# Performance work log

Measured on AMD Instinct MI355X. Metric: run time of the kernel, lower is better.

The kernel has to match this reference:

```python
import jax, jax.numpy as jnp
import numpy as np

B, C, H, W = 4, 256, 48, 48
HEADS, DH = 8, 64
HID = HEADS * DH
EPS = 1e-5
SCALE = DH ** -0.5


def setup_inputs() -> dict:
    key = jax.random.key(0)
    ks = jax.random.split(key, 8)
    return {
        "tensor": jax.random.normal(ks[0], (B, C, H, W), jnp.float32),
        "norm_g": jnp.ones((C,), jnp.float32),                      # ChanLayerNorm gamma
        "w_qkv": jax.random.normal(ks[1], (3 * HID, C), jnp.float32) * 0.02,  # 1x1 conv, no bias
        "dw_q": jax.random.normal(ks[2], (HID, 1, 3, 3), jnp.float32) * 0.1,  # depthwise 3x3
        "dw_k": jax.random.normal(ks[3], (HID, 1, 3, 3), jnp.float32) * 0.1,
        "dw_v": jax.random.normal(ks[4], (HID, 1, 3, 3), jnp.float32) * 0.1,
        "w_out": jax.random.normal(ks[5], (C, HID), jnp.float32) * 0.02,      # 1x1 conv out
        "b_out": jnp.zeros((C,), jnp.float32),
    }


def _rope(t):
    # t: (b, h, s, d) -- rotary embedding over flattened spatial positions
    s, d = t.shape[-2], t.shape[-1]
    inv_freq = 1.0 / (10000.0 ** (jnp.arange(0, d, 2, dtype=jnp.float32) / d))
    freqs = jnp.arange(s, dtype=jnp.float32)[:, None] * inv_freq[None, :]     # (s, d/2)
    emb = jnp.concatenate([freqs, freqs], axis=-1)                            # (s, d)
    cos, sin = jnp.cos(emb), jnp.sin(emb)
    t1, t2 = t[..., : d // 2], t[..., d // 2 :]
    rot = jnp.concatenate([-t2, t1], axis=-1)
    return t * cos + rot * sin


def _dwconv(x, w):
    # depthwise 3x3, padding=1 (Primer conv), groups = channels
    return jax.lax.conv_general_dilated(
        x, w, window_strides=(1, 1), padding="SAME",
        feature_group_count=x.shape[1],
        dimension_numbers=("NCHW", "OIHW", "NCHW"))


def reference(tensor, norm_g, w_qkv, dw_q, dw_k, dw_v, w_out, b_out):
    x = tensor
    # ChanLayerNorm: normalize over channel dim
    mean = jnp.mean(x, axis=1, keepdims=True)
    var = jnp.var(x, axis=1, keepdims=True)
    xn = (x - mean) * jax.lax.rsqrt(var + EPS) * norm_g[None, :, None, None]
    # 1x1 conv to qkv
    qkv = jnp.einsum("bchw,oc->bohw", xn, w_qkv)
    q, k, v = jnp.split(qkv, 3, axis=1)
    q, k, v = _dwconv(q, dw_q), _dwconv(k, dw_k), _dwconv(v, dw_v)
    # b (h d) x y -> b h (x y) d
    def to_seq(t):
        b = t.shape[0]
        return t.reshape(b, HEADS, DH, H * W).transpose(0, 1, 3, 2)
    q, k, v = to_seq(q), to_seq(k), to_seq(v)
    q, k = _rope(q), _rope(k)
    q = q * SCALE
    sim = jnp.einsum("bhid,bhjd->bhij", q, k)
    attn = jax.nn.softmax(sim, axis=-1)
    out = jnp.einsum("bhij,bhjd->bhid", attn, v)
    # b h (x y) d -> b (h d) x y
    out = out.transpose(0, 1, 3, 2).reshape(out.shape[0], HID, H, W)
    return jnp.einsum("bchw,oc->bohw", out, w_out) + b_out[None, :, None, None]
```

## Files before the change

kernel.cpp:

```cpp
#include <hip/hip_runtime.h>
#include <math.h>

#define SS 2304
#define C_IN 256
#define HID 512
#define QKV3 1536
#define HEADS 8
#define DH 64
#define BATCH 4
#define EPSV 1e-5f
#define SCALEV 0.125f

typedef short s8v __attribute__((ext_vector_type(8)));
typedef float f4v __attribute__((ext_vector_type(4)));
typedef unsigned int u4v __attribute__((ext_vector_type(4)));
typedef unsigned int uint32;

static __device__ inline unsigned short f2bf(float x) {
    unsigned int u = __float_as_uint(x);
    u += 0x7fffu + ((u >> 16) & 1u);
    return (unsigned short)(u >> 16);
}
static __device__ inline float bf2f(unsigned short h) {
    return __uint_as_float((unsigned int)h << 16);
}
static __device__ inline f4v mm(s8v a, s8v b, f4v c) {
    return __builtin_amdgcn_mfma_f32_16x16x32_bf16(a, b, c, 0, 0, 0);
}
static __device__ inline s8v pk4(uint32 a, uint32 b, uint32 c, uint32 d) {
    u4v t; t[0] = a; t[1] = b; t[2] = c; t[3] = d;
    return __builtin_bit_cast(s8v, t);
}
static __device__ inline uint32 pk_rnd(float x) {
    unsigned int u = __float_as_uint(x);
    unsigned int uh = (u + (0x7fffu + ((u >> 16) & 1u))) & 0xffff0000u;
    float r = x - __uint_as_float(uh);
    return (uh >> 16) | (__float_as_uint(r) & 0xffff0000u);
}
static __device__ inline uint32 pk_trunc(float x) {
    unsigned int u = __float_as_uint(x);
    unsigned int h = u & 0xffff0000u;
    float r = x - __uint_as_float(h);
    return (h >> 16) | (__float_as_uint(r) & 0xffff0000u);
}
static __device__ inline uint32 rot16(uint32 u) { return (u >> 16) | (u << 16); }
static __device__ inline u4v rot16v(u4v u) {
    u4v r; r[0] = rot16(u[0]); r[1] = rot16(u[1]); r[2] = rot16(u[2]); r[3] = rot16(u[3]);
    return r;
}

__global__ void prep_wgint(const float* __restrict__ w, const float* __restrict__ g,
                           uint32* __restrict__ wgint, float* __restrict__ wsum) {
    __shared__ float red[256];
    int o = blockIdx.x, c = threadIdx.x;
    float v = w[o * C_IN + c] * g[c];
    wgint[o * C_IN + c] = pk_rnd(v);
    red[c] = v;
    __syncthreads();
    for (int st = 128; st > 0; st >>= 1) {
        if (c < st) red[c] += red[c + st];
        __syncthreads();
    }
    if (c == 0) wsum[o] = red[0];
}

__global__ void prep_woutint(const float* __restrict__ w, uint32* __restrict__ wi) {
    int idx = blockIdx.x * 256 + threadIdx.x;
    wi[idx] = pk_rnd(w[idx]);
}

__global__ void prep_rope(float* __restrict__ cosT, float* __restrict__ sinT) {
    int idx = blockIdx.x * 256 + threadIdx.x;
    if (idx >= SS * 32) return;
    int s = idx >> 5, f = idx & 31;
    double inv = pow(10000.0, -(double)f / 32.0);
    double ang = (double)s * inv;
    cosT[idx] = (float)cos(ang);
    sinT[idx] = (float)sin(ang);
}

__global__ __launch_bounds__(256) void xt_pack(const float* __restrict__ x,
                                               uint32* __restrict__ xTint,
                                               float* __restrict__ psum,
                                               float* __restrict__ psq) {
    __shared__ float tile[64][65];
    __shared__ float sred[4][64];
    __shared__ float qred[4][64];
    int b = blockIdx.z;
    int c0 = blockIdx.y * 64;
    int s0 = blockIdx.x * 64;
    int t = threadIdx.x;
    int sl = t & 63, cg = t >> 6;
    float ps = 0.f, pq = 0.f;
#pragma unroll
    for (int i = 0; i < 16; ++i) {
        int c = cg * 16 + i;
        float v = x[((size_t)b * C_IN + c0 + c) * SS + s0 + sl];
        tile[c][sl] = v;
        ps += v;
        pq += v * v;
    }
    sred[cg][sl] = ps;
    qred[cg][sl] = pq;
    __syncthreads();
    int cl = t & 63, sg = t >> 6;
#pragma unroll
    for (int i = 0; i < 16; ++i) {
        int s = sg * 16 + i;
        xTint[((size_t)b * SS + s0 + s) * C_IN + c0 + cl] = pk_rnd(tile[cl][s]);
    }
    if (t < 64) {
        float S = (sred[0][t] + sred[1][t]) + (sred[2][t] + sred[3][t]);
        float Q = (qred[0][t] + qred[1][t]) + (qred[2][t] + qred[3][t]);
        size_t o = (size_t)blockIdx.y * (BATCH * SS) + (size_t)b * SS + s0 + t;
        psum[o] = S;
        psq[o] = Q;
    }
}

__global__ void finalize_stats(const float* __restrict__ psum,
                               const float* __restrict__ psq,
                               float* __restrict__ mean, float* __restrict__ rstd) {
    int p = blockIdx.x * 256 + threadIdx.x;
    const int NP = BATCH * SS;
    float S = (psum[p] + psum[NP + p]) + (psum[2 * NP + p] + psum[3 * NP + p]);
    float Q = (psq[p] + psq[NP + p]) + (psq[2 * NP + p] + psq[3 * NP + p]);
    float mu = S * (1.0f / C_IN);
    float var = Q * (1.0f / C_IN) - mu * mu;
    mean[p] = mu;
    rstd[p] = rsqrtf(var + EPSV);
}

__global__ __launch_bounds__(256, 4) void qkv_mfma(
    const uint32* __restrict__ wgint, const uint32* __restrict__ xTint,
    const float* __restrict__ wsum, const float* __restrict__ mean,
    const float* __restrict__ rstd, float* __restrict__ qkv) {
    int b = blockIdx.z;
    int m0 = blockIdx.y * 128;
    int n0 = blockIdx.x * 64;
    int t = threadIdx.x;
    int wv = t >> 6, lane = t & 63, l15 = lane & 15, quad = lane >> 4;
    int wm = wv * 32;
    const uint32* Ab = wgint + (size_t)(m0 + wm) * C_IN;
    const uint32* Bb = xTint + ((size_t)b * SS + n0) * C_IN;
    f4v acc[2][4];
#pragma unroll
    for (int mt = 0; mt < 2; ++mt)
#pragma unroll
        for (int nt = 0; nt < 4; ++nt) acc[mt][nt] = (f4v){0.f, 0.f, 0.f, 0.f};
    u4v af[2][2], bf[2][4];
    auto ldA = [&](int ch, u4v* A) {
#pragma unroll
        for (int mt = 0; mt < 2; ++mt)
            A[mt] = *(const u4v*)(Ab + (size_t)(mt * 16 + l15) * C_IN + ch * 16 + quad * 4);
    };
    auto ldB = [&](int ch, u4v* B) {
#pragma unroll
        for (int nt = 0; nt < 4; ++nt)
            B[nt] = *(const u4v*)(Bb + (size_t)(nt * 16 + l15) * C_IN + ch * 16 + quad * 4);
    };
    ldA(0, af[0]);
    ldB(0, bf[0]);
#pragma unroll 2
    for (int ch = 0; ch < 16; ++ch) {
        int cur = ch & 1, nxt = cur ^ 1;
        if (ch + 1 < 16) { ldA(ch + 1, af[nxt]); ldB(ch + 1, bf[nxt]); }
        u4v br[4];
#pragma unroll
        for (int nt = 0; nt < 4; ++nt) br[nt] = rot16v(bf[cur][nt]);
#pragma unroll
        for (int mt = 0; mt < 2; ++mt) {
            s8v a = __builtin_bit_cast(s8v, af[cur][mt]);
#pragma unroll
            for (int nt = 0; nt < 4; ++nt) {
                acc[mt][nt] = mm(a, __builtin_bit_cast(s8v, bf[cur][nt]), acc[mt][nt]);
                acc[mt][nt] = mm(a, __builtin_bit_cast(s8v, br[nt]), acc[mt][nt]);
            }
        }
    }
    float mnv[4], rsv[4];
#pragma unroll
    for (int nt = 0; nt < 4; ++nt) {
        int n = n0 + nt * 16 + l15;
        mnv[nt] = mean[b * SS + n];
        rsv[nt] = rstd[b * SS + n];
    }
#pragma unroll
    for (int mt = 0; mt < 2; ++mt)
#pragma unroll
        for (int r = 0; r < 4; ++r) {
            int m = m0 + wm + mt * 16 + quad * 4 + r;
            float ws = wsum[m];
            float* dst = qkv + ((size_t)b * QKV3 + m) * SS + n0 + l15;
#pragma unroll
            for (int nt = 0; nt < 4; ++nt)
                dst[nt * 16] = rsv[nt] * (acc[mt][nt][r] - mnv[nt] * ws);
        }
}

__global__ __launch_bounds__(256) void conv_rope(
    const float* __restrict__ qkv, const float* __restrict__ dwq,
    const float* __restrict__ dwk, const float* __restrict__ dwv,
    const float* __restrict__ cosT, const float* __restrict__ sinT,
    unsigned short* __restrict__ qhi, unsigned short* __restrict__ qlo,
    unsigned short* __restrict__ khi, unsigned short* __restrict__ klo,
    uint32* __restrict__ vtint) {
    __shared__ float tile[64][65];
    int b = blockIdx.z;
    int part = blockIdx.y >> 3;
    int h = blockIdx.y & 7;
    int s0 = blockIdx.x * 64;
    int t = threadIdx.x;
    int sl = t & 63, dgrp = t >> 6;
    int s = s0 + sl;
    int y = s / 48, xx = s - y * 48;
    int bh = b * HEADS + h;
    const float* dw = (part == 0) ? dwq : (part == 1) ? dwk : dwv;
#pragma unroll
    for (int i = 0; i < 16; ++i) {
        int d = dgrp * 16 + i;
        int cch = part * HID + h * DH + d;
        const float* src = qkv + ((size_t)b * QKV3 + cch) * SS;
        const float* wp = dw + (h * DH + d) * 9;
        float acc = 0.f;
#pragma unroll
        for (int dy = -1; dy <= 1; ++dy) {
            int yy = y + dy;
            if (yy < 0 || yy >= 48) continue;
#pragma unroll
            for (int dx = -1; dx <= 1; ++dx) {
                int xv = xx + dx;
                if (xv < 0 || xv >= 48) continue;
                acc += wp[(dy + 1) * 3 + (dx + 1)] * src[yy * 48 + xv];
            }
        }
        if (part == 2) {
            size_t o = ((size_t)bh * DH + d) * SS + s;
            vtint[o] = pk_rnd(acc);
        } else {
            tile[d][sl] = acc;
        }
    }
    if (part == 2) return;
    __syncthreads();
    int d2 = t & 63, srow = t >> 6;
    unsigned short* hiA = (part == 0) ? qhi : khi;
    unsigned short* loA = (part == 0) ? qlo : klo;
#pragma unroll
    for (int i = 0; i < 16; ++i) {
        int sp = srow + 4 * i;
        float v0 = tile[d2][sp];
        float vp = tile[d2 ^ 32][sp];
        int f = d2 & 31;
        float cv = cosT[(s0 + sp) * 32 + f];
        float sv = sinT[(s0 + sp) * 32 + f];
        float rot = (d2 < 32) ? -vp : vp;
        float val = v0 * cv + rot * sv;
        if (part == 0) val *= SCALEV;
        size_t o = ((size_t)bh * SS + s0 + sp) * DH + d2;
        unsigned short hu = f2bf(val);
        hiA[o] = hu;
        loA[o] = f2bf(val - bf2f(hu));
    }
}

__global__ __launch_bounds__(256, 2) void attn_mfma(
    const unsigned short* __restrict__ qhi, const unsigned short* __restrict__ qlo,
    const unsigned short* __restrict__ khi, const unsigned short* __restrict__ klo,
    const uint32* __restrict__ vtint,
    float* __restrict__ Opart, float* __restrict__ lpart) {
    __shared__ float lds[2][64][68];
    __shared__ float lsl[4][64];
    int bh = blockIdx.z;
    int jh = blockIdx.y;
    int i0 = blockIdx.x * 64;
    int t = threadIdx.x;
    int wv = t >> 6;
    int lane = t & 63;
    int l15 = lane & 15;
    int quad = lane >> 4;

    s8v qf[4][4];
#pragma unroll
    for (int ig = 0; ig < 4; ++ig) {
        size_t qb = ((size_t)bh * SS + i0 + ig * 16 + l15) * DH + quad * 8;
        qf[ig][0] = *(const s8v*)(qhi + qb);
        qf[ig][1] = *(const s8v*)(qhi + qb + 32);
        qf[ig][2] = *(const s8v*)(qlo + qb);
        qf[ig][3] = *(const s8v*)(qlo + qb + 32);
    }
    f4v oacc[4][4];
#pragma unroll
    for (int dt = 0; dt < 4; ++dt)
#pragma unroll
        for (int ig = 0; ig < 4; ++ig) oacc[dt][ig] = (f4v){0.f, 0.f, 0.f, 0.f};
    float lsum[4] = {0.f, 0.f, 0.f, 0.f};

    const size_t kbh = (size_t)bh * SS * DH;
    const uint32* vbase = vtint + (size_t)bh * DH * SS;
    const int jbase = jh * 1152 + wv * 16;

    s8v kc[2][4], vc[2][4];
    auto ldK = [&](int s, s8v* K) {
        size_t row = kbh + (size_t)(jbase + s * 64 + l15) * DH + quad * 8;
        K[0] = *(const s8v*)(khi + row);
        K[1] = *(const s8v*)(khi + row + 32);
        K[2] = *(const s8v*)(klo + row);
        K[3] = *(const s8v*)(klo + row + 32);
    };
    auto ldV = [&](int s, s8v* V) {
        size_t col = (size_t)(jbase + s * 64 + quad * 4);
#pragma unroll
        for (int dt = 0; dt < 4; ++dt)
            V[dt] = __builtin_bit_cast(
                s8v, *(const u4v*)(vbase + (size_t)(dt * 16 + l15) * SS + col));
    };
    ldK(0, kc[0]);
    ldV(0, vc[0]);
#pragma unroll 2
    for (int s = 0; s < 18; ++s) {
        int cur = s & 1, nxt = cur ^ 1;
        if (s + 1 < 18) { ldK(s + 1, kc[nxt]); ldV(s + 1, vc[nxt]); }
        f4v sv[4];
#pragma unroll
        for (int ig = 0; ig < 4; ++ig) {
            f4v sx = {0.f, 0.f, 0.f, 0.f};
            sx = mm(kc[cur][0], qf[ig][0], sx);
            sx = mm(kc[cur][1], qf[ig][1], sx);
            sx = mm(kc[cur][0], qf[ig][2], sx);
            sx = mm(kc[cur][1], qf[ig][3], sx);
            sx = mm(kc[cur][2], qf[ig][0], sx);
            sx = mm(kc[cur][3], qf[ig][1], sx);
            sv[ig] = sx;
        }
        s8v B1[4], B2[4];
#pragma unroll
        for (int ig = 0; ig < 4; ++ig) {
            float p0 = __expf(sv[ig][0]), p1 = __expf(sv[ig][1]);
            float p2 = __expf(sv[ig][2]), p3 = __expf(sv[ig][3]);
            lsum[ig] += (p0 + p1) + (p2 + p3);
            uint32 u0 = pk_trunc(p0), u1 = pk_trunc(p1);
            uint32 u2 = pk_trunc(p2), u3 = pk_trunc(p3);
            B1[ig] = pk4(u0, u1, u2, u3);
            B2[ig] = pk4(rot16(u0), rot16(u1), rot16(u2), rot16(u3));
        }
#pragma unroll
        for (int dt = 0; dt < 4; ++dt)
#pragma unroll
            for (int ig = 0; ig < 4; ++ig) {
                oacc[dt][ig] = mm(vc[cur][dt], B1[ig], oacc[dt][ig]);
                oacc[dt][ig] = mm(vc[cur][dt], B2[ig], oacc[dt][ig]);
            }
    }
#pragma unroll
    for (int ig = 0; ig < 4; ++ig) {
        float v = lsum[ig];
        v += __shfl_xor(v, 16);
        v += __shfl_xor(v, 32);
        if (quad == 0) lsl[wv][ig * 16 + l15] = v;
    }
    if (wv < 2) {
#pragma unroll
        for (int dt = 0; dt < 4; ++dt)
#pragma unroll
            for (int ig = 0; ig < 4; ++ig)
#pragma unroll
                for (int r = 0; r < 4; ++r)
                    lds[wv][dt * 16 + quad * 4 + r][ig * 16 + l15] = oacc[dt][ig][r];
    }
    __syncthreads();
    if (wv >= 2) {
#pragma unroll
        for (int dt = 0; dt < 4; ++dt)
#pragma unroll
            for (int ig = 0; ig < 4; ++ig)
#pragma unroll
                for (int r = 0; r < 4; ++r)
                    lds[wv - 2][dt * 16 + quad * 4 + r][ig * 16 + l15] += oacc[dt][ig][r];
    }
    __syncthreads();
    int d = t >> 2, qg = (t & 3) * 16;
    size_t ob = (((size_t)jh * 32 + bh) * DH + d) * SS + i0 + qg;
#pragma unroll
    for (int j4 = 0; j4 < 4; ++j4) {
        float4 a0 = *(const float4*)&lds[0][d][qg + j4 * 4];
        float4 a1 = *(const float4*)&lds[1][d][qg + j4 * 4];
        float4 rr;
        rr.x = a0.x + a1.x;
        rr.y = a0.y + a1.y;
        rr.z = a0.z + a1.z;
        rr.w = a0.w + a1.w;
        *(float4*)(Opart + ob + j4 * 4) = rr;
    }
    if (t < 64) {
        float v = (lsl[0][t] + lsl[1][t]) + (lsl[2][t] + lsl[3][t]);
        lpart[((size_t)jh * 32 + bh) * SS + i0 + t] = v;
    }
}

__global__ __launch_bounds__(256) void combine_t(
    const float* __restrict__ Opart, const float* __restrict__ lpart,
    uint32* __restrict__ OTint) {
    __shared__ uint32 tile[64][65];
    int bh = blockIdx.y;
    int s0 = blockIdx.x * 64;
    int b = bh >> 3, h = bh & 7;
    int t = threadIdx.x;
    int sl = t & 63, dg = t >> 6;
    float linv = 1.f / (lpart[(size_t)bh * SS + s0 + sl] +
                        lpart[(size_t)(32 + bh) * SS + s0 + sl]);
#pragma unroll
    for (int i = 0; i < 16; ++i) {
        int d = dg * 16 + i;
        size_t off = ((size_t)bh * DH + d) * SS + s0 + sl;
        float v = (Opart[off] + Opart[off + (size_t)32 * DH * SS]) * linv;
        tile[d][sl] = pk_rnd(v);
    }
    __syncthreads();
    int dl = t & 63, sg = t >> 6;
#pragma unroll
    for (int i = 0; i < 16; ++i) {
        int s = sg * 16 + i;
        OTint[((size_t)b * SS + s0 + s) * HID + h * DH + dl] = tile[dl][s];
    }
}

__global__ __launch_bounds__(256, 4) void outproj_mfma(
    const uint32* __restrict__ OTint, const uint32* __restrict__ woutint,
    const float* __restrict__ b_out, float* __restrict__ out) {
    int b = blockIdx.z;
    int m0 = blockIdx.y * 32;
    int n0 = blockIdx.x * 128;
    int t = threadIdx.x;
    int wv = t >> 6, lane = t & 63, l15 = lane & 15, quad = lane >> 4;
    int wn = wv * 32;
    const uint32* Ab = woutint + (size_t)m0 * HID;
    const uint32* Bb = OTint + ((size_t)b * SS + n0 + wn) * HID;
    f4v acc[2][2];
#pragma unroll
    for (int mt = 0; mt < 2; ++mt)
#pragma unroll
        for (int nt = 0; nt < 2; ++nt) acc[mt][nt] = (f4v){0.f, 0.f, 0.f, 0.f};
    u4v af[2][2], bf[2][2];
    auto ldA = [&](int ch, u4v* A) {
#pragma unroll
        for (int mt = 0; mt < 2; ++mt)
            A[mt] = *(const u4v*)(Ab + (size_t)(mt * 16 + l15) * HID + ch * 16 + quad * 4);
    };
    auto ldB = [&](int ch, u4v* B) {
#pragma unroll
        for (int nt = 0; nt < 2; ++nt)
            B[nt] = *(const u4v*)(Bb + (size_t)(nt * 16 + l15) * HID + ch * 16 + quad * 4);
    };
    ldA(0, af[0]);
    ldB(0, bf[0]);
#pragma unroll 2
    for (int ch = 0; ch < 32; ++ch) {
        int cur = ch & 1, nxt = cur ^ 1;
        if (ch + 1 < 32) { ldA(ch + 1, af[nxt]); ldB(ch + 1, bf[nxt]); }
        u4v br[2];
#pragma unroll
        for (int nt = 0; nt < 2; ++nt) br[nt] = rot16v(bf[cur][nt]);
#pragma unroll
        for (int mt = 0; mt < 2; ++mt) {
            s8v a = __builtin_bit_cast(s8v, af[cur][mt]);
#pragma unroll
            for (int nt = 0; nt < 2; ++nt) {
                acc[mt][nt] = mm(a, __builtin_bit_cast(s8v, bf[cur][nt]), acc[mt][nt]);
                acc[mt][nt] = mm(a, __builtin_bit_cast(s8v, br[nt]), acc[mt][nt]);
            }
        }
    }
#pragma unroll
    for (int mt = 0; mt < 2; ++mt)
#pragma unroll
        for (int r = 0; r < 4; ++r) {
            int o = m0 + mt * 16 + quad * 4 + r;
            float bo = b_out[o];
            float* dst = out + ((size_t)b * C_IN + o) * SS + n0 + wn + l15;
#pragma unroll
            for (int nt = 0; nt < 2; ++nt) dst[nt * 16] = acc[mt][nt][r] + bo;
        }
}

extern "C" void kernel_launch(void* const* d_in, const int* in_sizes, int n_in,
                              void* d_out, int out_size, void* d_ws, size_t ws_size,
                              hipStream_t stream) {
    (void)in_sizes; (void)n_in; (void)out_size; (void)ws_size;
    const float* x     = (const float*)d_in[0];
    const float* g     = (const float*)d_in[1];
    const float* w_qkv = (const float*)d_in[2];
    const float* dwq   = (const float*)d_in[3];
    const float* dwk   = (const float*)d_in[4];
    const float* dwv   = (const float*)d_in[5];
    const float* w_out = (const float*)d_in[6];
    const float* b_out = (const float*)d_in[7];
    float* out = (float*)d_out;

    char* ws = (char*)d_ws;
    size_t off = 0;
    auto alloc = [&](size_t nbytes) -> void* {
        char* p = ws + off;
        off = (off + nbytes + 255) & ~(size_t)255;
        return (void*)p;
    };
    const size_t NSD = (size_t)BATCH * HEADS * SS * DH;
    uint32* wgint   = (uint32*)alloc((size_t)QKV3 * C_IN * 4);
    uint32* woutint = (uint32*)alloc((size_t)C_IN * HID * 4);
    float* wsum = (float*)alloc((size_t)QKV3 * 4);
    float* mean = (float*)alloc((size_t)BATCH * SS * 4);
    float* rstd = (float*)alloc((size_t)BATCH * SS * 4);
    float* psum = (float*)alloc((size_t)4 * BATCH * SS * 4);
    float* psq  = (float*)alloc((size_t)4 * BATCH * SS * 4);
    float* cosT = (float*)alloc((size_t)SS * 32 * 4);
    float* sinT = (float*)alloc((size_t)SS * 32 * 4);
    float* qkv  = (float*)alloc((size_t)BATCH * QKV3 * SS * 4);
    unsigned short* qhi  = (unsigned short*)alloc(NSD * 2);
    unsigned short* qlo  = (unsigned short*)alloc(NSD * 2);
    unsigned short* khi  = (unsigned short*)alloc(NSD * 2);
    unsigned short* klo  = (unsigned short*)alloc(NSD * 2);
    uint32* vtint = (uint32*)alloc(NSD * 4);
    float* lpart = (float*)alloc((size_t)2 * 32 * SS * 4);
    uint32* xTint = (uint32*)qhi;
    float*  Opart = qkv;
    uint32* OTint = (uint32*)(qkv + 2 * NSD);

    prep_wgint<<<QKV3, 256, 0, stream>>>(w_qkv, g, wgint, wsum);
    prep_woutint<<<512, 256, 0, stream>>>(w_out, woutint);
    prep_rope<<<288, 256, 0, stream>>>(cosT, sinT);
    xt_pack<<<dim3(36, 4, BATCH), 256, 0, stream>>>(x, xTint, psum, psq);
    finalize_stats<<<36, 256, 0, stream>>>(psum, psq, mean, rstd);
    qkv_mfma<<<dim3(36, 12, BATCH), 256, 0, stream>>>(wgint, xTint, wsum, mean, rstd, qkv);
    conv_rope<<<dim3(36, 24, BATCH), 256, 0, stream>>>(qkv, dwq, dwk, dwv, cosT, sinT,
                                                       qhi, qlo, khi, klo, vtint);
    attn_mfma<<<dim3(36, 2, 32), 256, 0, stream>>>(qhi, qlo, khi, klo, vtint,
                                                   Opart, lpart);
    combine_t<<<dim3(36, 32), 256, 0, stream>>>(Opart, lpart, OTint);
    outproj_mfma<<<dim3(18, 8, BATCH), 256, 0, stream>>>(OTint, woutint, b_out, out);
}
```

Before: 481.1 us.

## Split attention waves into 2x2 query/key groups to cut registers and raise occupancy

Each wave now handles 32 queries over a 32-key slice instead of 64 queries over a 16-key slice, which halves the query fragments and output accumulators held per wave. K/V prefetch changes from a double buffer to single buffers reloaded right after use. Launch bounds rise from 2 to 3 blocks per SM, and LDS use for the reduction shrinks. The aim is higher occupancy to hide latency, at the cost of less explicit load/compute overlap and more K/V loads per query.

New measurement: 670.4 us. 39.4% more time.

```diff
diff --git a/kernel.cpp b/kernel.cpp
--- a/kernel.cpp
+++ b/kernel.cpp
@@ -264,13 +264,13 @@
     }
 }
 
-__global__ __launch_bounds__(256, 2) void attn_mfma(
+__global__ __launch_bounds__(256, 3) void attn_mfma(
     const unsigned short* __restrict__ qhi, const unsigned short* __restrict__ qlo,
     const unsigned short* __restrict__ khi, const unsigned short* __restrict__ klo,
     const uint32* __restrict__ vtint,
     float* __restrict__ Opart, float* __restrict__ lpart) {
-    __shared__ float lds[2][64][68];
-    __shared__ float lsl[4][64];
+    __shared__ float lds[2][64][36];
+    __shared__ float lsl[4][32];
     int bh = blockIdx.z;
     int jh = blockIdx.y;
     int i0 = blockIdx.x * 64;
@@ -279,121 +279,124 @@
     int lane = t & 63;
     int l15 = lane & 15;
     int quad = lane >> 4;
-
-    s8v qf[4][4];
-#pragma unroll
-    for (int ig = 0; ig < 4; ++ig) {
-        size_t qb = ((size_t)bh * SS + i0 + ig * 16 + l15) * DH + quad * 8;
+    int qg = wv >> 1;
+    int ks = wv & 1;
+
+    s8v qf[2][4];
+#pragma unroll
+    for (int ig = 0; ig < 2; ++ig) {
+        size_t qb = ((size_t)bh * SS + i0 + qg * 32 + ig * 16 + l15) * DH + quad * 8;
         qf[ig][0] = *(const s8v*)(qhi + qb);
         qf[ig][1] = *(const s8v*)(qhi + qb + 32);
         qf[ig][2] = *(const s8v*)(qlo + qb);
         qf[ig][3] = *(const s8v*)(qlo + qb + 32);
     }
-    f4v oacc[4][4];
+    f4v oacc[4][2];
 #pragma unroll
     for (int dt = 0; dt < 4; ++dt)
 #pragma unroll
-        for (int ig = 0; ig < 4; ++ig) oacc[dt][ig] = (f4v){0.f, 0.f, 0.f, 0.f};
-    float lsum[4] = {0.f, 0.f, 0.f, 0.f};
+        for (int ig = 0; ig < 2; ++ig) oacc[dt][ig] = (f4v){0.f, 0.f, 0.f, 0.f};
+    float lsum[2] = {0.f, 0.f};
 
     const size_t kbh = (size_t)bh * SS * DH;
     const uint32* vbase = vtint + (size_t)bh * DH * SS;
-    const int jbase = jh * 1152 + wv * 16;
+    const int jb0 = jh * 1152 + ks * 32;
 
     s8v kc[2][4], vc[2][4];
-    auto ldK = [&](int s, s8v* K) {
-        size_t row = kbh + (size_t)(jbase + s * 64 + l15) * DH + quad * 8;
-        K[0] = *(const s8v*)(khi + row);
-        K[1] = *(const s8v*)(khi + row + 32);
-        K[2] = *(const s8v*)(klo + row);
-        K[3] = *(const s8v*)(klo + row + 32);
-    };
-    auto ldV = [&](int s, s8v* V) {
-        size_t col = (size_t)(jbase + s * 64 + quad * 4);
-#pragma unroll
-        for (int dt = 0; dt < 4; ++dt)
-            V[dt] = __builtin_bit_cast(
-                s8v, *(const u4v*)(vbase + (size_t)(dt * 16 + l15) * SS + col));
-    };
-    ldK(0, kc[0]);
-    ldV(0, vc[0]);
-#pragma unroll 2
+    auto ldK = [&](int s) {
+#pragma unroll
+        for (int kt = 0; kt < 2; ++kt) {
+            size_t row = kbh + (size_t)(jb0 + s * 64 + kt * 16 + l15) * DH + quad * 8;
+            kc[kt][0] = *(const s8v*)(khi + row);
+            kc[kt][1] = *(const s8v*)(khi + row + 32);
+            kc[kt][2] = *(const s8v*)(klo + row);
+            kc[kt][3] = *(const s8v*)(klo + row + 32);
+        }
+    };
+    auto ldV = [&](int s) {
+#pragma unroll
+        for (int kt = 0; kt < 2; ++kt) {
+            size_t col = (size_t)(jb0 + s * 64 + kt * 16 + quad * 4);
+#pragma unroll
+            for (int dt = 0; dt < 4; ++dt)
+                vc[kt][dt] = __builtin_bit_cast(
+                    s8v, *(const u4v*)(vbase + (size_t)(dt * 16 + l15) * SS + col));
+        }
+    };
+    ldK(0);
+    ldV(0);
     for (int s = 0; s < 18; ++s) {
-        int cur = s & 1, nxt = cur ^ 1;
-        if (s + 1 < 18) { ldK(s + 1, kc[nxt]); ldV(s + 1, vc[nxt]); }
-        f4v sv[4];
-#pragma unroll
-        for (int ig = 0; ig < 4; ++ig) {
-            f4v sx = {0.f, 0.f, 0.f, 0.f};
-            sx = mm(kc[cur][0], qf[ig][0], sx);
-            sx = mm(kc[cur][1], qf[ig][1], sx);
-            sx = mm(kc[cur][0], qf[ig][2], sx);
-            sx = mm(kc[cur][1], qf[ig][3], sx);
-            sx = mm(kc[cur][2], qf[ig][0], sx);
-            sx = mm(kc[cur][3], qf[ig][1], sx);
-            sv[ig] = sx;
-        }
-        s8v B1[4], B2[4];
-#pragma unroll
-        for (int ig = 0; ig < 4; ++ig) {
-            float p0 = __expf(sv[ig][0]), p1 = __expf(sv[ig][1]);
-            float p2 = __expf(sv[ig][2]), p3 = __expf(sv[ig][3]);
-            lsum[ig] += (p0 + p1) + (p2 + p3);
-            uint32 u0 = pk_trunc(p0), u1 = pk_trunc(p1);
-            uint32 u2 = pk_trunc(p2), u3 = pk_trunc(p3);
-            B1[ig] = pk4(u0, u1, u2, u3);
-            B2[ig] = pk4(rot16(u0), rot16(u1), rot16(u2), rot16(u3));
-        }
-#pragma unroll
-        for (int dt = 0; dt < 4; ++dt)
-#pragma unroll
-            for (int ig = 0; ig < 4; ++ig) {
-                oacc[dt][ig] = mm(vc[cur][dt], B1[ig], oacc[dt][ig]);
-                oacc[dt][ig] = mm(vc[cur][dt], B2[ig], oacc[dt][ig]);
+        f4v sv[2][2];
+#pragma unroll
+        for (int kt = 0; kt < 2; ++kt)
+#pragma unroll
+            for (int ig = 0; ig < 2; ++ig) {
+                f4v sx = {0.f, 0.f, 0.f, 0.f};
+                sx = mm(kc[kt][0], qf[ig][0], sx);
+                sx = mm(kc[kt][1], qf[ig][1], sx);
+                sx = mm(kc[kt][0], qf[ig][2], sx);
+                sx = mm(kc[kt][1], qf[ig][3], sx);
+                sx = mm(kc[kt][2], qf[ig][0], sx);
+                sx = mm(kc[kt][3], qf[ig][1], sx);
+                sv[kt][ig] = sx;
             }
-    }
-#pragma unroll
-    for (int ig = 0; ig < 4; ++ig) {
+        if (s + 1 < 18) ldK(s + 1);
+#pragma unroll
+        for (int kt = 0; kt < 2; ++kt)
+#pragma unroll
+            for (int ig = 0; ig < 2; ++ig) {
+                float p0 = __expf(sv[kt][ig][0]), p1 = __expf(sv[kt][ig][1]);
+                float p2 = __expf(sv[kt][ig][2]), p3 = __expf(sv[kt][ig][3]);
+                lsum[ig] += (p0 + p1) + (p2 + p3);
+                uint32 u0 = pk_trunc(p0), u1 = pk_trunc(p1);
+                uint32 u2 = pk_trunc(p2), u3 = pk_trunc(p3);
+                s8v B1 = pk4(u0, u1, u2, u3);
+                s8v B2 = pk4(rot16(u0), rot16(u1), rot16(u2), rot16(u3));
+#pragma unroll
+                for (int dt = 0; dt < 4; ++dt) {
+                    oacc[dt][ig] = mm(vc[kt][dt], B1, oacc[dt][ig]);
+                    oacc[dt][ig] = mm(vc[kt][dt], B2, oacc[dt][ig]);
+                }
+            }
+        if (s + 1 < 18) ldV(s + 1);
+    }
+#pragma unroll
+    for (int ig = 0; ig < 2; ++ig) {
         float v = lsum[ig];
         v += __shfl_xor(v, 16);
         v += __shfl_xor(v, 32);
         if (quad == 0) lsl[wv][ig * 16 + l15] = v;
     }
-    if (wv < 2) {
+    if (ks == 0) {
 #pragma unroll
         for (int dt = 0; dt < 4; ++dt)
 #pragma unroll
-            for (int ig = 0; ig < 4; ++ig)
+            for (int ig = 0; ig < 2; ++ig)
 #pragma unroll
                 for (int r = 0; r < 4; ++r)
-                    lds[wv][dt * 16 + quad * 4 + r][ig * 16 + l15] = oacc[dt][ig][r];
+                    lds[qg][dt * 16 + quad * 4 + r][ig * 16 + l15] = oacc[dt][ig][r];
     }
     __syncthreads();
-    if (wv >= 2) {
+    if (ks == 1) {
 #pragma unroll
         for (int dt = 0; dt < 4; ++dt)
 #pragma unroll
-            for (int ig = 0; ig < 4; ++ig)
+            for (int ig = 0; ig < 2; ++ig)
 #pragma unroll
                 for (int r = 0; r < 4; ++r)
-                    lds[wv - 2][dt * 16 + quad * 4 + r][ig * 16 + l15] += oacc[dt][ig][r];
+                    lds[qg][dt * 16 + quad * 4 + r][ig * 16 + l15] += oacc[dt][ig][r];
     }
     __syncthreads();
-    int d = t >> 2, qg = (t & 3) * 16;
-    size_t ob = (((size_t)jh * 32 + bh) * DH + d) * SS + i0 + qg;
+    int d = t >> 2, qb4 = (t & 3) * 16;
+    size_t ob = (((size_t)jh * 32 + bh) * DH + d) * SS + i0 + qb4;
 #pragma unroll
     for (int j4 = 0; j4 < 4; ++j4) {
-        float4 a0 = *(const float4*)&lds[0][d][qg + j4 * 4];
-        float4 a1 = *(const float4*)&lds[1][d][qg + j4 * 4];
-        float4 rr;
-        rr.x = a0.x + a1.x;
-        rr.y = a0.y + a1.y;
-        rr.z = a0.z + a1.z;
-        rr.w = a0.w + a1.w;
-        *(float4*)(Opart + ob + j4 * 4) = rr;
+        int q = qb4 + j4 * 4;
+        *(float4*)(Opart + ob + j4 * 4) = *(const float4*)&lds[q >> 5][d][q & 31];
     }
     if (t < 64) {
-        float v = (lsl[0][t] + lsl[1][t]) + (lsl[2][t] + lsl[3][t]);
+        int qg2 = t >> 5, idx = t & 31;
+        float v = lsl[qg2 * 2][idx] + lsl[qg2 * 2 + 1][idx];
         lpart[((size_t)jh * 32 + bh) * SS + i0 + t] = v;
     }
 }
```

## Stage Q fragments in LDS to raise attention occupancy; pack qkv intermediate

Applied to the files above, without the earlier changes.

The attention kernel no longer keeps all Q hi/lo fragments in registers. It stages them in a shared LDS buffer, which is reused for the output reduction after an extra barrier, and raises the launch bound from 2 to 3 blocks per CU to cut register pressure and improve latency hiding. Separately, qkv_mfma now stores its output as a packed hi/lo bf16 pair in a uint32, and conv_rope unpacks it. That changes how values are represented but does not shrink storage. The cost is extra LDS reads inside the inner loop, plus pack/unpack ALU work and a small precision difference.

Result: slower. 1.124 ms (+133.6%).

```diff
diff --git a/kernel.cpp b/kernel.cpp
--- a/kernel.cpp
+++ b/kernel.cpp
@@ -42,6 +42,9 @@
     unsigned int h = u & 0xffff0000u;
     float r = x - __uint_as_float(h);
     return (h >> 16) | (__float_as_uint(r) & 0xffff0000u);
+}
+static __device__ inline float unpk(uint32 u) {
+    return __uint_as_float(u << 16) + __uint_as_float(u & 0xffff0000u);
 }
 static __device__ inline uint32 rot16(uint32 u) { return (u >> 16) | (u << 16); }
 static __device__ inline u4v rot16v(u4v u) {
@@ -134,7 +137,7 @@
 __global__ __launch_bounds__(256, 4) void qkv_mfma(
     const uint32* __restrict__ wgint, const uint32* __restrict__ xTint,
     const float* __restrict__ wsum, const float* __restrict__ mean,
-    const float* __restrict__ rstd, float* __restrict__ qkv) {
+    const float* __restrict__ rstd, uint32* __restrict__ qkvint) {
     int b = blockIdx.z;
     int m0 = blockIdx.y * 128;
     int n0 = blockIdx.x * 64;
@@ -191,15 +194,15 @@
         for (int r = 0; r < 4; ++r) {
             int m = m0 + wm + mt * 16 + quad * 4 + r;
             float ws = wsum[m];
-            float* dst = qkv + ((size_t)b * QKV3 + m) * SS + n0 + l15;
+            uint32* dst = qkvint + ((size_t)b * QKV3 + m) * SS + n0 + l15;
 #pragma unroll
             for (int nt = 0; nt < 4; ++nt)
-                dst[nt * 16] = rsv[nt] * (acc[mt][nt][r] - mnv[nt] * ws);
+                dst[nt * 16] = pk_rnd(rsv[nt] * (acc[mt][nt][r] - mnv[nt] * ws));
         }
 }
 
 __global__ __launch_bounds__(256) void conv_rope(
-    const float* __restrict__ qkv, const float* __restrict__ dwq,
+    const uint32* __restrict__ qkvint, const float* __restrict__ dwq,
     const float* __restrict__ dwk, const float* __restrict__ dwv,
     const float* __restrict__ cosT, const float* __restrict__ sinT,
     unsigned short* __restrict__ qhi, unsigned short* __restrict__ qlo,
@@ -220,7 +223,7 @@
     for (int i = 0; i < 16; ++i) {
         int d = dgrp * 16 + i;
         int cch = part * HID + h * DH + d;
-        const float* src = qkv + ((size_t)b * QKV3 + cch) * SS;
+        const uint32* src = qkvint + ((size_t)b * QKV3 + cch) * SS;
         const float* wp = dw + (h * DH + d) * 9;
         float acc = 0.f;
 #pragma unroll
@@ -231,7 +234,7 @@
             for (int dx = -1; dx <= 1; ++dx) {
                 int xv = xx + dx;
                 if (xv < 0 || xv >= 48) continue;
-                acc += wp[(dy + 1) * 3 + (dx + 1)] * src[yy * 48 + xv];
+                acc += wp[(dy + 1) * 3 + (dx + 1)] * unpk(src[yy * 48 + xv]);
             }
         }
         if (part == 2) {
@@ -264,13 +267,15 @@
     }
 }
 
-__global__ __launch_bounds__(256, 2) void attn_mfma(
+__global__ __launch_bounds__(256, 3) void attn_mfma(
     const unsigned short* __restrict__ qhi, const unsigned short* __restrict__ qlo,
     const unsigned short* __restrict__ khi, const unsigned short* __restrict__ klo,
     const uint32* __restrict__ vtint,
     float* __restrict__ Opart, float* __restrict__ lpart) {
-    __shared__ float lds[2][64][68];
-    __shared__ float lsl[4][64];
+    __shared__ __align__(16) char smem[34816 + 1024];
+    unsigned short (*qs)[64][72] = (unsigned short (*)[64][72])smem;
+    float (*ldsO)[64][68] = (float (*)[64][68])smem;
+    float (*lsl)[64] = (float (*)[64])(smem + 34816);
     int bh = blockIdx.z;
     int jh = blockIdx.y;
     int i0 = blockIdx.x * 64;
@@ -280,15 +285,19 @@
     int l15 = lane & 15;
     int quad = lane >> 4;
 
-    s8v qf[4][4];
-#pragma unroll
-    for (int ig = 0; ig < 4; ++ig) {
-        size_t qb = ((size_t)bh * SS + i0 + ig * 16 + l15) * DH + quad * 8;
-        qf[ig][0] = *(const s8v*)(qhi + qb);
-        qf[ig][1] = *(const s8v*)(qhi + qb + 32);
-        qf[ig][2] = *(const s8v*)(qlo + qb);
-        qf[ig][3] = *(const s8v*)(qlo + qb + 32);
-    }
+    {
+        int row = t >> 3;
+        int col = (t & 7) * 8;
+#pragma unroll
+        for (int rr = 0; rr < 2; ++rr) {
+            int q = row + rr * 32;
+            size_t gb = ((size_t)bh * SS + i0 + q) * DH + col;
+            *(s8v*)&qs[0][q][col] = *(const s8v*)(qhi + gb);
+            *(s8v*)&qs[1][q][col] = *(const s8v*)(qlo + gb);
+        }
+    }
+    __syncthreads();
+
     f4v oacc[4][4];
 #pragma unroll
     for (int dt = 0; dt < 4; ++dt)
@@ -324,13 +333,18 @@
         f4v sv[4];
 #pragma unroll
         for (int ig = 0; ig < 4; ++ig) {
+            int qrow = ig * 16 + l15;
+            s8v qh0 = *(const s8v*)&qs[0][qrow][quad * 8];
+            s8v qh1 = *(const s8v*)&qs[0][qrow][32 + quad * 8];
+            s8v ql0 = *(const s8v*)&qs[1][qrow][quad * 8];
+            s8v ql1 = *(const s8v*)&qs[1][qrow][32 + quad * 8];
             f4v sx = {0.f, 0.f, 0.f, 0.f};
-            sx = mm(kc[cur][0], qf[ig][0], sx);
-            sx = mm(kc[cur][1], qf[ig][1], sx);
-            sx = mm(kc[cur][0], qf[ig][2], sx);
-            sx = mm(kc[cur][1], qf[ig][3], sx);
-            sx = mm(kc[cur][2], qf[ig][0], sx);
-            sx = mm(kc[cur][3], qf[ig][1], sx);
+            sx = mm(kc[cur][0], qh0, sx);
+            sx = mm(kc[cur][1], qh1, sx);
+            sx = mm(kc[cur][0], ql0, sx);
+            sx = mm(kc[cur][1], ql1, sx);
+            sx = mm(kc[cur][2], qh0, sx);
+            sx = mm(kc[cur][3], qh1, sx);
             sv[ig] = sx;
         }
         s8v B1[4], B2[4];
@@ -352,13 +366,18 @@
                 oacc[dt][ig] = mm(vc[cur][dt], B2[ig], oacc[dt][ig]);
             }
     }
+    float lred[4];
 #pragma unroll
     for (int ig = 0; ig < 4; ++ig) {
         float v = lsum[ig];
         v += __shfl_xor(v, 16);
         v += __shfl_xor(v, 32);
-        if (quad == 0) lsl[wv][ig * 16 + l15] = v;
-    }
+        lred[ig] = v;
+    }
+    __syncthreads();
+#pragma unroll
+    for (int ig = 0; ig < 4; ++ig)
+        if (quad == 0) lsl[wv][ig * 16 + l15] = lred[ig];
     if (wv < 2) {
 #pragma unroll
         for (int dt = 0; dt < 4; ++dt)
@@ -366,7 +385,7 @@
             for (int ig = 0; ig < 4; ++ig)
 #pragma unroll
                 for (int r = 0; r < 4; ++r)
-                    lds[wv][dt * 16 + quad * 4 + r][ig * 16 + l15] = oacc[dt][ig][r];
+                    ldsO[wv][dt * 16 + quad * 4 + r][ig * 16 + l15] = oacc[dt][ig][r];
     }
     __syncthreads();
     if (wv >= 2) {
@@ -376,15 +395,15 @@
             for (int ig = 0; ig < 4; ++ig)
 #pragma unroll
                 for (int r = 0; r < 4; ++r)
-                    lds[wv - 2][dt * 16 + quad * 4 + r][ig * 16 + l15] += oacc[dt][ig][r];
+                    ldsO[wv - 2][dt * 16 + quad * 4 + r][ig * 16 + l15] += oacc[dt][ig][r];
     }
     __syncthreads();
     int d = t >> 2, qg = (t & 3) * 16;
     size_t ob = (((size_t)jh * 32 + bh) * DH + d) * SS + i0 + qg;
 #pragma unroll
     for (int j4 = 0; j4 < 4; ++j4) {
-        float4 a0 = *(const float4*)&lds[0][d][qg + j4 * 4];
-        float4 a1 = *(const float4*)&lds[1][d][qg + j4 * 4];
+        float4 a0 = *(const float4*)&ldsO[0][d][qg + j4 * 4];
+        float4 a1 = *(const float4*)&ldsO[1][d][qg + j4 * 4];
         float4 rr;
         rr.x = a0.x + a1.x;
         rr.y = a0.y + a1.y;
@@ -514,24 +533,26 @@
     float* psq  = (float*)alloc((size_t)4 * BATCH * SS * 4);
     float* cosT = (float*)alloc((size_t)SS * 32 * 4);
     float* sinT = (float*)alloc((size_t)SS * 32 * 4);
-    float* qkv  = (float*)alloc((size_t)BATCH * QKV3 * SS * 4);
+    char* scratchA = (char*)alloc((size_t)3 * NSD * 4);
     unsigned short* qhi  = (unsigned short*)alloc(NSD * 2);
     unsigned short* qlo  = (unsigned short*)alloc(NSD * 2);
     unsigned short* khi  = (unsigned short*)alloc(NSD * 2);
     unsigned short* klo  = (unsigned short*)alloc(NSD * 2);
     uint32* vtint = (uint32*)alloc(NSD * 4);
     float* lpart = (float*)alloc((size_t)2 * 32 * SS * 4);
-    uint32* xTint = (uint32*)qhi;
-    float*  Opart = qkv;
-    uint32* OTint = (uint32*)(qkv + 2 * NSD);
+    uint32* xTint  = (uint32*)qhi;
+    uint32* qkvint = (uint32*)scratchA;
+    float*  Opart  = (float*)scratchA;
+    uint32* OTint  = (uint32*)(scratchA + (size_t)2 * NSD * 4);
 
     prep_wgint<<<QKV3, 256, 0, stream>>>(w_qkv, g, wgint, wsum);
     prep_woutint<<<512, 256, 0, stream>>>(w_out, woutint);
     prep_rope<<<288, 256, 0, stream>>>(cosT, sinT);
     xt_pack<<<dim3(36, 4, BATCH), 256, 0, stream>>>(x, xTint, psum, psq);
     finalize_stats<<<36, 256, 0, stream>>>(psum, psq, mean, rstd);
-    qkv_mfma<<<dim3(36, 12, BATCH), 256, 0, stream>>>(wgint, xTint, wsum, mean, rstd, qkv);
-    conv_rope<<<dim3(36, 24, BATCH), 256, 0, stream>>>(qkv, dwq, dwk, dwv, cosT, sinT,
+    qkv_mfma<<<dim3(36, 12, BATCH), 256, 0, stream>>>(wgint, xTint, wsum, mean, rstd,
+                                                      qkvint);
+    conv_rope<<<dim3(36, 24, BATCH), 256, 0, stream>>>(qkvint, dwq, dwk, dwv, cosT, sinT,
                                                        qhi, qlo, khi, klo, vtint);
     attn_mfma<<<dim3(36, 2, 32), 256, 0, stream>>>(qhi, qlo, khi, klo, vtint,
                                                    Opart, lpart);
```

## Drop attention KV split, fuse combine into attention, pack qkv intermediate

Applied to the files above, without the earlier changes.

Removes the two-way key split in the attention kernel so each block walks the full key range and normalises and transposes its output directly, which eliminates the combine kernel and the partial O/l buffers. The qkv projection output is stored as a packed hi/lo bf16 pair instead of fp32 and unpacked in the depthwise conv. The three prep kernels are merged into one launch. This halves the attention grid (1152 blocks at 2 per CU), so there is less parallelism in exchange for less memory traffic and fewer launches.

New measurement: 477.2 us. No clear change (-0.8%).

```diff
diff --git a/kernel.cpp b/kernel.cpp
--- a/kernel.cpp
+++ b/kernel.cpp
@@ -43,40 +43,44 @@
     float r = x - __uint_as_float(h);
     return (h >> 16) | (__float_as_uint(r) & 0xffff0000u);
 }
+static __device__ inline float unpk(uint32 u) {
+    return __uint_as_float(u << 16) + __uint_as_float(u & 0xffff0000u);
+}
 static __device__ inline uint32 rot16(uint32 u) { return (u >> 16) | (u << 16); }
 static __device__ inline u4v rot16v(u4v u) {
     u4v r; r[0] = rot16(u[0]); r[1] = rot16(u[1]); r[2] = rot16(u[2]); r[3] = rot16(u[3]);
     return r;
 }
 
-__global__ void prep_wgint(const float* __restrict__ w, const float* __restrict__ g,
-                           uint32* __restrict__ wgint, float* __restrict__ wsum) {
+__global__ void prep_all(const float* __restrict__ w_qkv, const float* __restrict__ g,
+                         uint32* __restrict__ wgint, float* __restrict__ wsum,
+                         const float* __restrict__ w_out, uint32* __restrict__ woutint,
+                         float* __restrict__ cosT, float* __restrict__ sinT) {
     __shared__ float red[256];
-    int o = blockIdx.x, c = threadIdx.x;
-    float v = w[o * C_IN + c] * g[c];
-    wgint[o * C_IN + c] = pk_rnd(v);
-    red[c] = v;
-    __syncthreads();
-    for (int st = 128; st > 0; st >>= 1) {
-        if (c < st) red[c] += red[c + st];
+    int bid = blockIdx.x;
+    int t = threadIdx.x;
+    if (bid < QKV3) {
+        int o = bid, c = t;
+        float v = w_qkv[o * C_IN + c] * g[c];
+        wgint[o * C_IN + c] = pk_rnd(v);
+        red[c] = v;
         __syncthreads();
-    }
-    if (c == 0) wsum[o] = red[0];
-}
-
-__global__ void prep_woutint(const float* __restrict__ w, uint32* __restrict__ wi) {
-    int idx = blockIdx.x * 256 + threadIdx.x;
-    wi[idx] = pk_rnd(w[idx]);
-}
-
-__global__ void prep_rope(float* __restrict__ cosT, float* __restrict__ sinT) {
-    int idx = blockIdx.x * 256 + threadIdx.x;
-    if (idx >= SS * 32) return;
-    int s = idx >> 5, f = idx & 31;
-    double inv = pow(10000.0, -(double)f / 32.0);
-    double ang = (double)s * inv;
-    cosT[idx] = (float)cos(ang);
-    sinT[idx] = (float)sin(ang);
+        for (int st = 128; st > 0; st >>= 1) {
+            if (c < st) red[c] += red[c + st];
+            __syncthreads();
+        }
+        if (c == 0) wsum[o] = red[0];
+    } else if (bid < QKV3 + 512) {
+        int idx = (bid - QKV3) * 256 + t;
+        woutint[idx] = pk_rnd(w_out[idx]);
+    } else {
+        int idx = (bid - QKV3 - 512) * 256 + t;
+        int s = idx >> 5, f = idx & 31;
+        double inv = pow(10000.0, -(double)f / 32.0);
+        double ang = (double)s * inv;
+        cosT[idx] = (float)cos(ang);
+        sinT[idx] = (float)sin(ang);
+    }
 }
 
 __global__ __launch_bounds__(256) void xt_pack(const float* __restrict__ x,
@@ -134,7 +138,7 @@
 __global__ __launch_bounds__(256, 4) void qkv_mfma(
     const uint32* __restrict__ wgint, const uint32* __restrict__ xTint,
     const float* __restrict__ wsum, const float* __restrict__ mean,
-    const float* __restrict__ rstd, float* __restrict__ qkv) {
+    const float* __restrict__ rstd, uint32* __restrict__ qkvint) {
     int b = blockIdx.z;
     int m0 = blockIdx.y * 128;
     int n0 = blockIdx.x * 64;
@@ -191,15 +195,15 @@
         for (int r = 0; r < 4; ++r) {
             int m = m0 + wm + mt * 16 + quad * 4 + r;
             float ws = wsum[m];
-            float* dst = qkv + ((size_t)b * QKV3 + m) * SS + n0 + l15;
+            uint32* dst = qkvint + ((size_t)b * QKV3 + m) * SS + n0 + l15;
 #pragma unroll
             for (int nt = 0; nt < 4; ++nt)
-                dst[nt * 16] = rsv[nt] * (acc[mt][nt][r] - mnv[nt] * ws);
+                dst[nt * 16] = pk_rnd(rsv[nt] * (acc[mt][nt][r] - mnv[nt] * ws));
         }
 }
 
 __global__ __launch_bounds__(256) void conv_rope(
-    const float* __restrict__ qkv, const float* __restrict__ dwq,
+    const uint32* __restrict__ qkvint, const float* __restrict__ dwq,
     const float* __restrict__ dwk, const float* __restrict__ dwv,
     const float* __restrict__ cosT, const float* __restrict__ sinT,
     unsigned short* __restrict__ qhi, unsigned short* __restrict__ qlo,
@@ -220,7 +224,7 @@
     for (int i = 0; i < 16; ++i) {
         int d = dgrp * 16 + i;
         int cch = part * HID + h * DH + d;
-        const float* src = qkv + ((size_t)b * QKV3 + cch) * SS;
+        const uint32* src = qkvint + ((size_t)b * QKV3 + cch) * SS;
         const float* wp = dw + (h * DH + d) * 9;
         float acc = 0.f;
 #pragma unroll
@@ -231,7 +235,7 @@
             for (int dx = -1; dx <= 1; ++dx) {
                 int xv = xx + dx;
                 if (xv < 0 || xv >= 48) continue;
-                acc += wp[(dy + 1) * 3 + (dx + 1)] * src[yy * 48 + xv];
+                acc += wp[(dy + 1) * 3 + (dx + 1)] * unpk(src[yy * 48 + xv]);
             }
         }
         if (part == 2) {
@@ -267,12 +271,10 @@
 __global__ __launch_bounds__(256, 2) void attn_mfma(
     const unsigned short* __restrict__ qhi, const unsigned short* __restrict__ qlo,
     const unsigned short* __restrict__ khi, const unsigned short* __restrict__ klo,
-    const uint32* __restrict__ vtint,
-    float* __restrict__ Opart, float* __restrict__ lpart) {
+    const uint32* __restrict__ vtint, uint32* __restrict__ OTint) {
     __shared__ float lds[2][64][68];
     __shared__ float lsl[4][64];
-    int bh = blockIdx.z;
-    int jh = blockIdx.y;
+    int bh = blockIdx.y;
     int i0 = blockIdx.x * 64;
     int t = threadIdx.x;
     int wv = t >> 6;
@@ -298,7 +300,7 @@
 
     const size_t kbh = (size_t)bh * SS * DH;
     const uint32* vbase = vtint + (size_t)bh * DH * SS;
-    const int jbase = jh * 1152 + wv * 16;
+    const int jbase = wv * 16;
 
     s8v kc[2][4], vc[2][4];
     auto ldK = [&](int s, s8v* K) {
@@ -318,9 +320,9 @@
     ldK(0, kc[0]);
     ldV(0, vc[0]);
 #pragma unroll 2
-    for (int s = 0; s < 18; ++s) {
+    for (int s = 0; s < 36; ++s) {
         int cur = s & 1, nxt = cur ^ 1;
-        if (s + 1 < 18) { ldK(s + 1, kc[nxt]); ldV(s + 1, vc[nxt]); }
+        if (s + 1 < 36) { ldK(s + 1, kc[nxt]); ldV(s + 1, vc[nxt]); }
         f4v sv[4];
 #pragma unroll
         for (int ig = 0; ig < 4; ++ig) {
@@ -379,50 +381,20 @@
                     lds[wv - 2][dt * 16 + quad * 4 + r][ig * 16 + l15] += oacc[dt][ig][r];
     }
     __syncthreads();
-    int d = t >> 2, qg = (t & 3) * 16;
-    size_t ob = (((size_t)jh * 32 + bh) * DH + d) * SS + i0 + qg;
-#pragma unroll
-    for (int j4 = 0; j4 < 4; ++j4) {
-        float4 a0 = *(const float4*)&lds[0][d][qg + j4 * 4];
-        float4 a1 = *(const float4*)&lds[1][d][qg + j4 * 4];
-        float4 rr;
-        rr.x = a0.x + a1.x;
-        rr.y = a0.y + a1.y;
-        rr.z = a0.z + a1.z;
-        rr.w = a0.w + a1.w;
-        *(float4*)(Opart + ob + j4 * 4) = rr;
-    }
-    if (t < 64) {
-        float v = (lsl[0][t] + lsl[1][t]) + (lsl[2][t] + lsl[3][t]);
-        lpart[((size_t)jh * 32 + bh) * SS + i0 + t] = v;
-    }
-}
-
-__global__ __launch_bounds__(256) void combine_t(
-    const float* __restrict__ Opart, const float* __restrict__ lpart,
-    uint32* __restrict__ OTint) {
-    __shared__ uint32 tile[64][65];
-    int bh = blockIdx.y;
-    int s0 = blockIdx.x * 64;
+    int q = t >> 2, dg = t & 3;
+    float linv = 1.f / ((lsl[0][q] + lsl[1][q]) + (lsl[2][q] + lsl[3][q]));
     int b = bh >> 3, h = bh & 7;
-    int t = threadIdx.x;
-    int sl = t & 63, dg = t >> 6;
-    float linv = 1.f / (lpart[(size_t)bh * SS + s0 + sl] +
-                        lpart[(size_t)(32 + bh) * SS + s0 + sl]);
-#pragma unroll
-    for (int i = 0; i < 16; ++i) {
-        int d = dg * 16 + i;
-        size_t off = ((size_t)bh * DH + d) * SS + s0 + sl;
-        float v = (Opart[off] + Opart[off + (size_t)32 * DH * SS]) * linv;
-        tile[d][sl] = pk_rnd(v);
-    }
-    __syncthreads();
-    int dl = t & 63, sg = t >> 6;
-#pragma unroll
-    for (int i = 0; i < 16; ++i) {
-        int s = sg * 16 + i;
-        OTint[((size_t)b * SS + s0 + s) * HID + h * DH + dl] = tile[dl][s];
-    }
+    uint32* dst = OTint + ((size_t)b * SS + i0 + q) * HID + h * DH + dg * 16;
+    u4v ov[4];
+#pragma unroll
+    for (int j4 = 0; j4 < 4; ++j4)
+#pragma unroll
+        for (int i = 0; i < 4; ++i) {
+            int d = dg * 16 + j4 * 4 + i;
+            ov[j4][i] = pk_rnd((lds[0][d][q] + lds[1][d][q]) * linv);
+        }
+#pragma unroll
+    for (int j4 = 0; j4 < 4; ++j4) *(u4v*)(dst + j4 * 4) = ov[j4];
 }
 
 __global__ __launch_bounds__(256, 4) void outproj_mfma(
@@ -514,27 +486,24 @@
     float* psq  = (float*)alloc((size_t)4 * BATCH * SS * 4);
     float* cosT = (float*)alloc((size_t)SS * 32 * 4);
     float* sinT = (float*)alloc((size_t)SS * 32 * 4);
-    float* qkv  = (float*)alloc((size_t)BATCH * QKV3 * SS * 4);
+    char* scratchA = (char*)alloc((size_t)3 * NSD * 4);
     unsigned short* qhi  = (unsigned short*)alloc(NSD * 2);
     unsigned short* qlo  = (unsigned short*)alloc(NSD * 2);
     unsigned short* khi  = (unsigned short*)alloc(NSD * 2);
     unsigned short* klo  = (unsigned short*)alloc(NSD * 2);
     uint32* vtint = (uint32*)alloc(NSD * 4);
-    float* lpart = (float*)alloc((size_t)2 * 32 * SS * 4);
-    uint32* xTint = (uint32*)qhi;
-    float*  Opart = qkv;
-    uint32* OTint = (uint32*)(qkv + 2 * NSD);
-
-    prep_wgint<<<QKV3, 256, 0, stream>>>(w_qkv, g, wgint, wsum);
-    prep_woutint<<<512, 256, 0, stream>>>(w_out, woutint);
-    prep_rope<<<288, 256, 0, stream>>>(cosT, sinT);
+    uint32* xTint  = (uint32*)qhi;
+    uint32* qkvint = (uint32*)scratchA;
+    uint32* OTint  = (uint32*)scratchA;
+
+    prep_all<<<QKV3 + 512 + 288, 256, 0, stream>>>(w_qkv, g, wgint, wsum,
+                                                   w_out, woutint, cosT, sinT);
     xt_pack<<<dim3(36, 4, BATCH), 256, 0, stream>>>(x, xTint, psum, psq);
     finalize_stats<<<36, 256, 0, stream>>>(psum, psq, mean, rstd);
-    qkv_mfma<<<dim3(36, 12, BATCH), 256, 0, stream>>>(wgint, xTint, wsum, mean, rstd, qkv);
-    conv_rope<<<dim3(36, 24, BATCH), 256, 0, stream>>>(qkv, dwq, dwk, dwv, cosT, sinT,
+    qkv_mfma<<<dim3(36, 12, BATCH), 256, 0, stream>>>(wgint, xTint, wsum, mean, rstd,
+                                                      qkvint);
+    conv_rope<<<dim3(36, 24, BATCH), 256, 0, stream>>>(qkvint, dwq, dwk, dwv, cosT, sinT,
                                                        qhi, qlo, khi, klo, vtint);
-    attn_mfma<<<dim3(36, 2, 32), 256, 0, stream>>>(qhi, qlo, khi, klo, vtint,
-                                                   Opart, lpart);
-    combine_t<<<dim3(36, 32), 256, 0, stream>>>(Opart, lpart, OTint);
+    attn_mfma<<<dim3(36, 32), 256, 0, stream>>>(qhi, qlo, khi, klo, vtint, OTint);
     outproj_mfma<<<dim3(18, 8, BATCH), 256, 0, stream>>>(OTint, woutint, b_out, out);
 }
```
